# Optimization experiments

Hardware: AMD Instinct MI355X
Metric: run time of the kernel (lower is better)

## Reference

```python
import jax, jax.numpy as jnp
import numpy as np

D_MODEL = 2048
NUM_HEADS = 16
D_K = D_MODEL // NUM_HEADS
THETA = 10000.0
MAX_SEQ_LEN = 2048
B, S = 2, 2048


def setup_inputs() -> dict:
    key = jax.random.key(0)
    ks = jax.random.split(key, 5)
    x = jax.random.normal(ks[0], (B, S, D_MODEL), dtype=jnp.float32)
    token_positions = jnp.tile(jnp.arange(S, dtype=jnp.int64 if jax.config.jax_enable_x64 else jnp.int32), (B, 1))
    wq = jax.random.normal(ks[1], (D_MODEL, D_MODEL), dtype=jnp.float32)
    wk = jax.random.normal(ks[2], (D_MODEL, D_MODEL), dtype=jnp.float32)
    wv = jax.random.normal(ks[3], (D_MODEL, D_MODEL), dtype=jnp.float32)
    wo = jax.random.normal(ks[4], (D_MODEL, D_MODEL), dtype=jnp.float32)
    return {"x": x, "token_positions": token_positions, "wq": wq, "wk": wk, "wv": wv, "wo": wo}


def _rope_tables():
    # inv freqs: exp(arange(0,d_k,2) * (-log(theta)/d_k))  -> [d_k/2]
    inv_freq = jnp.exp(jnp.arange(0, D_K, 2, dtype=jnp.float32) * (-np.log(THETA) / D_K))
    m = jnp.arange(MAX_SEQ_LEN, dtype=jnp.float32)[:, None]  # [L,1]
    ang = m * inv_freq[None, :]                               # [L, d_k/2]
    return jnp.cos(ang), jnp.sin(ang)


def _apply_rope(x, token_positions, cos_tab, sin_tab):
    # x: [B, H, S, d_k]; token_positions: [B, S]
    cos = cos_tab[token_positions][:, None, :, :]  # [B,1,S,d_k/2]
    sin = sin_tab[token_positions][:, None, :, :]
    xe = x[..., 0::2]
    xo = x[..., 1::2]
    re = xe * cos - xo * sin
    ro = xo * cos + xe * sin
    out = jnp.stack([re, ro], axis=-1).reshape(x.shape)
    return out


def reference(x, token_positions, wq, wk, wv, wo):
    b, s, _ = x.shape
    cos_tab, sin_tab = _rope_tables()

    def split_heads(t):  # [B,S,D] -> [B,H,S,d_k]
        return t.reshape(b, s, NUM_HEADS, D_K).transpose(0, 2, 1, 3)

    q = _apply_rope(split_heads(x @ wq), token_positions, cos_tab, sin_tab)
    k = _apply_rope(split_heads(x @ wk), token_positions, cos_tab, sin_tab)
    v = split_heads(x @ wv)

    scores = jnp.einsum("bhqd,bhkd->bhqk", q, k) / jnp.sqrt(jnp.float32(D_K))
    causal = jnp.tril(jnp.ones((s, s), dtype=bool))
    scores = jnp.where(causal[None, None], scores, jnp.float32(-1e9))
    attn = jax.nn.softmax(scores, axis=-1)
    out = jnp.einsum("bhqk,bhkd->bhqd", attn, v)
    out = out.transpose(0, 2, 1, 3).reshape(b, s, D_MODEL)
    return out @ wo
```

## Files before the change

kernel.cpp:

```cpp
#include <hip/hip_runtime.h>
#include <hip/hip_bf16.h>
#include <cstdio>

namespace {

constexpr int kSeq = 2048;
constexpr int kDModel = 2048;
constexpr int kHeads = 16;
constexpr int kDk = 128;
constexpr int kBatch = 2;
constexpr int kM = kBatch * kSeq;
constexpr float kQScale = 0.08838834764831845f;

typedef __bf16 bf16_t;
typedef __bf16 bf16x8 __attribute__((ext_vector_type(8)));
typedef __bf16 bf16x4 __attribute__((ext_vector_type(4)));
typedef float f32x4 __attribute__((ext_vector_type(4)));
typedef short s16x4 __attribute__((ext_vector_type(4)));

__device__ __forceinline__ f32x4 mfma32(bf16x8 a, bf16x8 b, f32x4 c) {
  return __builtin_amdgcn_mfma_f32_16x16x32_bf16(a, b, c, 0, 0, 0);
}

#if __has_builtin(__builtin_amdgcn_mfma_f32_16x16x16_bf16)
__device__ __forceinline__ f32x4 mfma16(bf16x4 a, bf16x4 b, f32x4 c) {
  return __builtin_amdgcn_mfma_f32_16x16x16_bf16(a, b, c, 0, 0, 0);
}
#else
__device__ __forceinline__ f32x4 mfma16(bf16x4 a, bf16x4 b, f32x4 c) {
  union U { bf16x4 b; s16x4 s; } ua, ub;
  ua.b = a; ub.b = b;
  return __builtin_amdgcn_mfma_f32_16x16x16bf16_1k(ua.s, ub.s, c, 0, 0, 0);
}
#endif

using gas_void = const __attribute__((address_space(1))) void;
using las_void = __attribute__((address_space(3))) void;

__device__ __forceinline__ void gload_lds16(const bf16_t* g, bf16_t* l) {
  __builtin_amdgcn_global_load_lds((gas_void*)g, (las_void*)l, 16, 0, 0);
}

__global__ void k_rope_table(float* __restrict__ cost, float* __restrict__ sint) {
  const int p = blockIdx.x;
  const int i = threadIdx.x;
  const double inv = exp(-(double)(2 * i) * 9.210340371976184 / 128.0);
  const double ang = (double)p * inv;
  cost[p * 64 + i] = (float)cos(ang);
  sint[p * 64 + i] = (float)sin(ang);
}

__global__ void k_split_x(const float* __restrict__ x, bf16_t* __restrict__ xh,
                          bf16_t* __restrict__ xl, int n) {
  const int idx = (blockIdx.x * blockDim.x + threadIdx.x) * 4;
  if (idx >= n) return;
  const float4 v = *(const float4*)(x + idx);
  const float vv[4] = {v.x, v.y, v.z, v.w};
  bf16x4 hv, lv;
#pragma unroll
  for (int j = 0; j < 4; ++j) {
    const bf16_t h = (bf16_t)vv[j];
    hv[j] = h;
    lv[j] = (bf16_t)(vv[j] - (float)h);
  }
  *(bf16x4*)(xh + idx) = hv;
  *(bf16x4*)(xl + idx) = lv;
}

__global__ void k_transpose_w(const float* __restrict__ w, bf16_t* __restrict__ wth,
                              bf16_t* __restrict__ wtl) {
  __shared__ float tile[32][33];
  const int bx = blockIdx.x * 32;
  const int by = blockIdx.y * 32;
  const int tx = threadIdx.x, ty = threadIdx.y;
#pragma unroll
  for (int i = 0; i < 32; i += 8)
    tile[ty + i][tx] = w[(size_t)(by + ty + i) * kDModel + bx + tx];
  __syncthreads();
#pragma unroll
  for (int i = 0; i < 32; i += 8) {
    const float v = tile[tx][ty + i];
    const size_t o = (size_t)(bx + ty + i) * kDModel + by + tx;
    const bf16_t h = (bf16_t)v;
    wth[o] = h;
    if (wtl) wtl[o] = (bf16_t)(v - (float)h);
  }
}

__global__ __launch_bounds__(512, 2) void k_gemmqk(
    const bf16_t* __restrict__ Ah, const bf16_t* __restrict__ Al,
    const bf16_t* __restrict__ Bh, const bf16_t* __restrict__ Bl,
    bf16_t* __restrict__ Qh, bf16_t* __restrict__ Ql,
    bf16_t* __restrict__ Kh, bf16_t* __restrict__ Kl,
    const int* __restrict__ tokpos, const float* __restrict__ cost,
    const float* __restrict__ sint) {
  __shared__ __align__(16) bf16_t sA[3][512 * 32];
  __shared__ __align__(16) bf16_t sB[3][128 * 32];
  constexpr int ntk = 192;

  const int tid = threadIdx.x;
  const int wid = tid >> 6, lane = tid & 63;
  const int lo = lane & 15, hi = lane >> 4;
  const int wr = wid >> 1, wc = wid & 1;

  const int bid = blockIdx.x;
  const int wgid = (bid & 7) * 32 + (bid >> 3);
  const int mt = wgid >> 5, nt = wgid & 31;
  const int m0 = mt * 512, n0 = nt * 128;

  const int sr = tid >> 2;
  const int sc = ((tid & 3) ^ ((sr >> 1) & 3)) * 8;
  size_t offA[4];
#pragma unroll
  for (int ui = 0; ui < 4; ++ui)
    offA[ui] = (size_t)(m0 + ui * 128 + sr) * 2048 + sc;
  const size_t offB = (size_t)(n0 + sr) * 2048 + sc;
  const int ldsT = wid * 512;

  auto STAGE = [&](int slot, int tt) {
    const bf16_t *As, *Bs;
    int kb;
    if (tt < 64) {
      As = Ah; Bs = Bh; kb = tt * 32;
    } else if (tt < 128) {
      As = Ah; Bs = Bl; kb = (tt - 64) * 32;
    } else {
      As = Al; Bs = Bh; kb = (tt - 128) * 32;
    }
    bf16_t* dA = sA[slot] + ldsT;
#pragma unroll
    for (int ui = 0; ui < 4; ++ui)
      gload_lds16(As + offA[ui] + kb, dA + ui * 4096);
    gload_lds16(Bs + offB + kb, sB[slot] + ldsT);
  };

  const int xq = (lo >> 1) & 3;
  int aoff[8], boff[4];
#pragma unroll
  for (int mi = 0; mi < 8; ++mi)
    aoff[mi] = (wr * 128 + mi * 16 + lo) * 32 + ((hi ^ xq) * 8);
#pragma unroll
  for (int ni = 0; ni < 4; ++ni)
    boff[ni] = (wc * 64 + ni * 16 + lo) * 32 + ((hi ^ xq) * 8);

  f32x4 acc[8][4];
  const f32x4 z = {0.f, 0.f, 0.f, 0.f};
#pragma unroll
  for (int i = 0; i < 8; ++i)
#pragma unroll
    for (int j = 0; j < 4; ++j) acc[i][j] = z;

  STAGE(0, 0);
  STAGE(1, 1);
  asm volatile("s_waitcnt vmcnt(5)" ::: "memory");
  __builtin_amdgcn_s_barrier();
  __builtin_amdgcn_sched_barrier(0);

  int s0 = 0;
#pragma unroll 1
  for (int t = 0; t < ntk; ++t) {
    const bf16_t* sa = sA[s0];
    const bf16_t* sb = sB[s0];
    int s2 = s0 + 2;
    if (s2 >= 3) s2 -= 3;

    bf16x8 af[8], bfr[4];
#pragma unroll
    for (int mi = 0; mi < 4; ++mi) af[mi] = *(const bf16x8*)(sa + aoff[mi]);
#pragma unroll
    for (int ni = 0; ni < 4; ++ni) bfr[ni] = *(const bf16x8*)(sb + boff[ni]);
    if (t + 2 < ntk) STAGE(s2, t + 2);
#pragma unroll
    for (int mi = 4; mi < 8; ++mi) af[mi] = *(const bf16x8*)(sa + aoff[mi]);

    if (t + 3 < ntk)
      asm volatile("s_waitcnt vmcnt(5)" ::: "memory");
    else
      asm volatile("s_waitcnt vmcnt(0)" ::: "memory");
    asm volatile("s_waitcnt lgkmcnt(4)" ::: "memory");
    __builtin_amdgcn_s_barrier();
    __builtin_amdgcn_sched_barrier(0);

    __builtin_amdgcn_s_setprio(1);
#pragma unroll
    for (int ni = 0; ni < 4; ++ni)
#pragma unroll
      for (int mi = 0; mi < 4; ++mi)
        acc[mi][ni] = mfma32(af[mi], bfr[ni], acc[mi][ni]);
    __builtin_amdgcn_s_setprio(0);

    asm volatile("s_waitcnt lgkmcnt(0)" ::: "memory");
    __builtin_amdgcn_sched_barrier(0);
    __builtin_amdgcn_s_setprio(1);
#pragma unroll
    for (int ni = 0; ni < 4; ++ni)
#pragma unroll
      for (int mi = 4; mi < 8; ++mi)
        acc[mi][ni] = mfma32(af[mi], bfr[ni], acc[mi][ni]);
    __builtin_amdgcn_s_setprio(0);

    __builtin_amdgcn_s_barrier();
    __builtin_amdgcn_sched_barrier(0);

    s0 += 1;
    if (s0 >= 3) s0 = 0;
  }

  const int qk = n0 >> 11;
  bf16_t* Xh = qk ? Kh : Qh;
  bf16_t* Xl = qk ? Kl : Ql;
  const float scale = qk ? 1.0f : kQScale;
  const int is64 = (tokpos[1] == 0) ? 1 : 0;
#pragma unroll
  for (int mi = 0; mi < 8; ++mi) {
#pragma unroll
    for (int r = 0; r < 4; ++r) {
      const int row = m0 + wr * 128 + mi * 16 + hi * 4 + r;
      const int pos = is64 ? tokpos[2 * row] : tokpos[row];
#pragma unroll
      for (int ni = 0; ni < 4; ++ni) {
        const int col = n0 + wc * 64 + ni * 16 + lo;
        const float v = acc[mi][ni][r] * scale;
        const float pv = __shfl_xor(v, 1);
        const int ip = (col & 127) >> 1;
        const float c = cost[pos * 64 + ip];
        const float sn = sint[pos * 64 + ip];
        const float sgn = (lo & 1) ? sn : -sn;
        const float rv = v * c + pv * sgn;
        const bf16_t hb = (bf16_t)rv;
        const size_t o = (size_t)row * 2048 + (col & 2047);
        Xh[o] = hb;
        Xl[o] = (bf16_t)(rv - (float)hb);
      }
    }
  }
}

template <int EPI>
__global__ __launch_bounds__(512) void k_gemm8(
    const bf16_t* __restrict__ Ah, const bf16_t* __restrict__ Bh,
    void* __restrict__ O0, int NT, int ntk) {
  __shared__ __align__(16) bf16_t sA[3][256 * 64];
  __shared__ __align__(16) bf16_t sB[3][128 * 64];

  const int tid = threadIdx.x;
  const int wid = tid >> 6, lane = tid & 63;
  const int lo = lane & 15, hi = lane >> 4;
  const int wrr = wid >> 1, wcc = wid & 1;
  const int x7 = lo & 7;

  const int bid = blockIdx.x;
  const int wgid = (bid & 7) * (gridDim.x >> 3) + (bid >> 3);
  const int mt = wgid / NT, nt = wgid % NT;
  const int m0 = mt * 256, n0 = nt * 128;

  const int rB = tid >> 3;
  const int ch8 = ((tid & 7) ^ (rB & 7)) * 8;
  size_t offA[4], offB[2];
#pragma unroll
  for (int u = 0; u < 2; ++u)
#pragma unroll
    for (int i = 0; i < 2; ++i)
      offA[u * 2 + i] = (size_t)(m0 + u * 128 + i * 64 + rB) * 2048 + ch8;
#pragma unroll
  for (int i = 0; i < 2; ++i)
    offB[i] = (size_t)(n0 + i * 64 + rB) * 2048 + ch8;
  const int ldsOff = wid * 512;

  auto STAGE_A = [&](int slot, int t) {
    const bf16_t* base = Ah + t * 64;
    bf16_t* d = sA[slot] + ldsOff;
#pragma unroll
    for (int ui = 0; ui < 4; ++ui) gload_lds16(base + offA[ui], d + ui * 4096);
  };
  auto STAGE_B = [&](int slot, int t) {
    const bf16_t* base = Bh + t * 64;
    bf16_t* d = sB[slot] + ldsOff;
#pragma unroll
    for (int i = 0; i < 2; ++i) gload_lds16(base + offB[i], d + i * 4096);
  };

  int aoff[4][2], boff[4][2];
#pragma unroll
  for (int mi = 0; mi < 4; ++mi)
#pragma unroll
    for (int ks = 0; ks < 2; ++ks)
      aoff[mi][ks] = (wrr * 64 + mi * 16 + lo) * 64 + (((ks * 4 + hi) ^ x7) * 8);
#pragma unroll
  for (int ni = 0; ni < 4; ++ni)
#pragma unroll
    for (int ks = 0; ks < 2; ++ks)
      boff[ni][ks] = (wcc * 64 + ni * 16 + lo) * 64 + (((ks * 4 + hi) ^ x7) * 8);

  f32x4 acc[4][4];
  const f32x4 z = {0.f, 0.f, 0.f, 0.f};
#pragma unroll
  for (int i = 0; i < 4; ++i)
#pragma unroll
    for (int j = 0; j < 4; ++j) acc[i][j] = z;

  STAGE_A(0, 0);
  STAGE_B(0, 0);
  STAGE_A(1, 1);
  STAGE_B(1, 1);
  asm volatile("s_waitcnt vmcnt(6)" ::: "memory");
  __builtin_amdgcn_s_barrier();
  asm volatile("" ::: "memory");

  int s0 = 0;
  for (int t = 0; t < ntk; ++t) {
    const bf16_t* sa = sA[s0];
    const bf16_t* sb = sB[s0];
    int s2 = s0 + 2;
    if (s2 >= 3) s2 -= 3;
    const bool pf = (t + 2 < ntk);

    bf16x8 af[2][2], bfr[4][2];
#pragma unroll
    for (int mi = 0; mi < 2; ++mi)
#pragma unroll
      for (int ks = 0; ks < 2; ++ks)
        af[mi][ks] = *(const bf16x8*)(sa + aoff[mi][ks]);
#pragma unroll
    for (int ni = 0; ni < 4; ++ni)
#pragma unroll
      for (int ks = 0; ks < 2; ++ks)
        bfr[ni][ks] = *(const bf16x8*)(sb + boff[ni][ks]);
    if (pf) STAGE_A(s2, t + 2);
    asm volatile("" ::: "memory");
    __builtin_amdgcn_s_barrier();
    asm volatile("" ::: "memory");
    __builtin_amdgcn_s_setprio(1);
#pragma unroll
    for (int ni = 0; ni < 4; ++ni)
#pragma unroll
      for (int mi = 0; mi < 2; ++mi)
#pragma unroll
        for (int ks = 0; ks < 2; ++ks)
          acc[mi][ni] = mfma32(af[mi][ks], bfr[ni][ks], acc[mi][ni]);
    __builtin_amdgcn_s_setprio(0);

    bf16x8 ag[2][2];
#pragma unroll
    for (int mi = 0; mi < 2; ++mi)
#pragma unroll
      for (int ks = 0; ks < 2; ++ks)
        ag[mi][ks] = *(const bf16x8*)(sa + aoff[2 + mi][ks]);
    if (pf) STAGE_B(s2, t + 2);
    if (pf)
      asm volatile("s_waitcnt vmcnt(6)" ::: "memory");
    else
      asm volatile("s_waitcnt vmcnt(0)" ::: "memory");
    __builtin_amdgcn_s_barrier();
    asm volatile("" ::: "memory");
    __builtin_amdgcn_s_setprio(1);
#pragma unroll
    for (int ni = 0; ni < 4; ++ni)
#pragma unroll
      for (int mi = 0; mi < 2; ++mi)
#pragma unroll
        for (int ks = 0; ks < 2; ++ks)
          acc[2 + mi][ni] = mfma32(ag[mi][ks], bfr[ni][ks], acc[2 + mi][ni]);
    __builtin_amdgcn_s_setprio(0);

    s0 += 1;
    if (s0 >= 3) s0 = 0;
  }

  if constexpr (EPI == 0) {
    float* C = (float*)O0;
#pragma unroll
    for (int mi = 0; mi < 4; ++mi)
#pragma unroll
      for (int ni = 0; ni < 4; ++ni)
#pragma unroll
        for (int r = 0; r < 4; ++r) {
          const int row = m0 + wrr * 64 + mi * 16 + hi * 4 + r;
          const int col = n0 + wcc * 64 + ni * 16 + lo;
          C[(size_t)row * 2048 + col] = acc[mi][ni][r];
        }
  } else {
    bf16_t* VT = (bf16_t*)O0;
#pragma unroll
    for (int mi = 0; mi < 4; ++mi)
#pragma unroll
      for (int ni = 0; ni < 4; ++ni) {
        const int col = n0 + wcc * 64 + ni * 16 + lo;
        const int h = col >> 7, d = col & 127;
        const int rowb = m0 + wrr * 64 + mi * 16 + hi * 4;
        const int b = rowb >> 11, s = rowb & (kSeq - 1);
        bf16x4 ov;
#pragma unroll
        for (int r = 0; r < 4; ++r) ov[r] = (bf16_t)acc[mi][ni][r];
        *(bf16x4*)(VT + ((size_t)((b * kHeads + h) * kDk + d)) * kSeq + s) = ov;
      }
  }
}

__global__ __launch_bounds__(512, 2) void k_attn4(
    const bf16_t* __restrict__ Qh, const bf16_t* __restrict__ Ql,
    const bf16_t* __restrict__ Kh, const bf16_t* __restrict__ Kl,
    const bf16_t* __restrict__ VT, bf16_t* __restrict__ Ob) {
  __shared__ __align__(16) bf16_t sK[2][2][64 * 128];
  __shared__ __align__(16) bf16_t sV[2][128 * 64];

  const int tid = threadIdx.x;
  const int wid = tid >> 6, lane = tid & 63;
  const int lo = lane & 15, hi = lane >> 4;
  const int flat = blockIdx.x;
  const int j = flat >> 3;
  const int bh = (flat & 7) * 4 + (j & 3);
  const int p = j >> 2;
  const int b = bh >> 4, h = bh & 15;
  const int qiW = (wid < 4) ? (15 - p) : p;
  const int qw = qiW * 128 + (wid & 3) * 32;
  const int nkv = 2 * (15 - p) + 2;

  bf16x8 qhf[4][2], qlf[4][2];
  {
    const size_t qbase =
        (size_t)(b * kSeq + qw + lo) * kDModel + h * kDk + hi * 8;
#pragma unroll
    for (int qt = 0; qt < 2; ++qt)
#pragma unroll
      for (int ks = 0; ks < 4; ++ks) {
        const size_t o = qbase + (size_t)qt * 16 * kDModel + ks * 32;
        qhf[ks][qt] = *(const bf16x8*)(Qh + o);
        qlf[ks][qt] = *(const bf16x8*)(Ql + o);
      }
  }

  const int rK0 = wid * 8 + (lane >> 4);
  const int gK0 = ((lane & 15) ^ (rK0 & 15)) * 8;
  const int gK1 = ((lane & 15) ^ ((rK0 + 4) & 15)) * 8;
  const bf16_t* pKh0 = Kh + (size_t)(b * kSeq + rK0) * kDModel + h * kDk + gK0;
  const bf16_t* pKh1 = Kh + (size_t)(b * kSeq + rK0 + 4) * kDModel + h * kDk + gK1;
  const bf16_t* pKl0 = Kl + (pKh0 - Kh);
  const bf16_t* pKl1 = Kl + (pKh1 - Kh);
  const int dV0 = wid * 16 + (lane >> 3);
  const int gV0 = ((lane & 7) ^ (dV0 & 7)) * 8;
  const int gV1 = ((lane & 7) ^ ((dV0 + 8) & 7)) * 8;
  const bf16_t* pV0 = VT + (size_t)(bh * kDk + dV0) * kSeq + gV0;
  const bf16_t* pV1 = VT + (size_t)(bh * kDk + dV0 + 8) * kSeq + gV1;
  const int ldsK = (wid * 8) * 128;
  const int ldsV = (wid * 16) * 64;

  f32x4 of[8][2];
  const f32x4 z = {0.f, 0.f, 0.f, 0.f};
#pragma unroll
  for (int di = 0; di < 8; ++di) {
    of[di][0] = z;
    of[di][1] = z;
  }
  float m[2] = {-3e38f, -3e38f};
  float l[2] = {0.f, 0.f};

  auto STAGE = [&](int buf, int t) {
    const size_t ko = (size_t)t * 64 * kDModel;
    const size_t vo = (size_t)t * 64;
    bf16_t* dk = sK[buf][0] + ldsK;
    bf16_t* dl = sK[buf][1] + ldsK;
    gload_lds16(pKh0 + ko, dk);
    gload_lds16(pKh1 + ko, dk + 512);
    gload_lds16(pKl0 + ko, dl);
    gload_lds16(pKl1 + ko, dl + 512);
    bf16_t* dv = sV[buf] + ldsV;
    gload_lds16(pV0 + vo, dv);
    gload_lds16(pV1 + vo, dv + 512);
  };

  STAGE(0, 0);
  __syncthreads();

  for (int t = 0; t < nkv; ++t) {
    const int kv0 = t * 64;
    if (t + 1 < nkv) STAGE((t + 1) & 1, t + 1);

    if (kv0 <= qw + 31) {
      const bf16_t* bKh = sK[t & 1][0];
      const bf16_t* bKl = sK[t & 1][1];
      const bf16_t* bV = sV[t & 1];
      const bool maskedw = (kv0 + 63 > qw);

      f32x4 st[4][2];
#pragma unroll
      for (int kt = 0; kt < 4; ++kt) {
        st[kt][0] = z;
        st[kt][1] = z;
      }
#pragma unroll
      for (int kt = 0; kt < 4; ++kt) {
#pragma unroll
        for (int ks = 0; ks < 4; ++ks) {
          const int krow = kt * 16 + lo;
          const int ka = krow * 128 + (((ks * 4 + hi) ^ (krow & 15)) * 8);
          const bf16x8 kh8 = *(const bf16x8*)(bKh + ka);
          const bf16x8 kl8 = *(const bf16x8*)(bKl + ka);
#pragma unroll
          for (int qt = 0; qt < 2; ++qt) {
            st[kt][qt] = mfma32(kh8, qhf[ks][qt], st[kt][qt]);
            st[kt][qt] = mfma32(kh8, qlf[ks][qt], st[kt][qt]);
            st[kt][qt] = mfma32(kl8, qhf[ks][qt], st[kt][qt]);
          }
        }
      }

      bf16x4 pb[4][2];
#pragma unroll
      for (int qt = 0; qt < 2; ++qt) {
        const int q = qw + qt * 16 + lo;
        float mt = -3e38f;
#pragma unroll
        for (int kt = 0; kt < 4; ++kt)
#pragma unroll
          for (int r = 0; r < 4; ++r) {
            float s = st[kt][qt][r];
            if (maskedw && (kv0 + kt * 16 + hi * 4 + r > q)) s = -1e30f;
            st[kt][qt][r] = s;
            mt = fmaxf(mt, s);
          }
        mt = fmaxf(mt, __shfl_xor(mt, 16));
        mt = fmaxf(mt, __shfl_xor(mt, 32));
        if (!__all(mt <= m[qt] + 8.f)) {
          const float mnew = fmaxf(m[qt], mt);
          const float corr = __expf(m[qt] - mnew);
          l[qt] *= corr;
#pragma unroll
          for (int di = 0; di < 8; ++di) of[di][qt] = of[di][qt] * corr;
          m[qt] = mnew;
        }
        float rs = 0.f;
#pragma unroll
        for (int kt = 0; kt < 4; ++kt) {
          bf16x4 pv;
#pragma unroll
          for (int r = 0; r < 4; ++r) {
            const float pp = __expf(st[kt][qt][r] - m[qt]);
            rs += pp;
            pv[r] = (bf16_t)pp;
          }
          pb[kt][qt] = pv;
        }
        rs += __shfl_xor(rs, 16);
        rs += __shfl_xor(rs, 32);
        l[qt] += rs;
      }

#pragma unroll
      for (int di = 0; di < 8; ++di) {
        const int d = di * 16 + lo;
#pragma unroll
        for (int kt = 0; kt < 4; ++kt) {
          const int va =
              d * 64 + (((kt * 2 + (hi >> 1)) ^ (d & 7)) * 8) + (hi & 1) * 4;
          const bf16x4 vf = *(const bf16x4*)(bV + va);
          of[di][0] = mfma16(vf, pb[kt][0], of[di][0]);
          of[di][1] = mfma16(vf, pb[kt][1], of[di][1]);
        }
      }
    }
    __syncthreads();
  }

#pragma unroll
  for (int qt = 0; qt < 2; ++qt) {
    const float linv = 1.f / l[qt];
    const size_t ob =
        (size_t)(b * kSeq + qw + qt * 16 + lo) * kDModel + h * kDk + hi * 4;
#pragma unroll
    for (int di = 0; di < 8; ++di) {
      bf16x4 ov;
#pragma unroll
      for (int r = 0; r < 4; ++r) ov[r] = (bf16_t)(of[di][qt][r] * linv);
      *(bf16x4*)(Ob + ob + di * 16) = ov;
    }
  }
}

}

extern "C" void kernel_launch(void* const* d_in, const int* in_sizes, int n_in,
                              void* d_out, int out_size, void* d_ws, size_t ws_size,
                              hipStream_t stream) {
  (void)in_sizes; (void)n_in; (void)out_size;
  const float* x = (const float*)d_in[0];
  const int* tokpos = (const int*)d_in[1];
  const float* wq = (const float*)d_in[2];
  const float* wk = (const float*)d_in[3];
  const float* wv = (const float*)d_in[4];
  const float* wo = (const float*)d_in[5];
  float* out = (float*)d_out;

  char* p = (char*)d_ws;
  auto take = [&](size_t bytes) { char* q = p; p += bytes; return q; };
  float* cost = (float*)take((size_t)kSeq * 64 * sizeof(float));
  float* sint = (float*)take((size_t)kSeq * 64 * sizeof(float));
  const size_t mat = (size_t)kM * kDModel * sizeof(bf16_t);
  const size_t wmat = (size_t)kDModel * kDModel * sizeof(bf16_t);
  bf16_t* xh = (bf16_t*)take(mat);
  bf16_t* xl = (bf16_t*)take(mat);
  bf16_t* wqkth = (bf16_t*)take(2 * wmat);
  bf16_t* wqktl = (bf16_t*)take(2 * wmat);
  bf16_t* wvt = (bf16_t*)take(wmat);
  bf16_t* wot = (bf16_t*)take(wmat);
  bf16_t* qh = (bf16_t*)take(mat);
  bf16_t* ql = (bf16_t*)take(mat);
  bf16_t* kh = (bf16_t*)take(mat);
  bf16_t* kl = (bf16_t*)take(mat);
  bf16_t* vt = (bf16_t*)take(mat);
  bf16_t* ob = (bf16_t*)take(mat);
  if ((size_t)(p - (char*)d_ws) > ws_size) {
    fprintf(stderr, "MHA: workspace too small: need %zu have %zu\n",
            (size_t)(p - (char*)d_ws), ws_size);
    return;
  }

  k_rope_table<<<dim3(kSeq), dim3(64), 0, stream>>>(cost, sint);
  k_split_x<<<dim3((kM * kDModel) / (256 * 4)), dim3(256), 0, stream>>>(
      x, xh, xl, kM * kDModel);
  {
    dim3 tb(32, 8), tg(kDModel / 32, kDModel / 32);
    k_transpose_w<<<tg, tb, 0, stream>>>(wq, wqkth, wqktl);
    k_transpose_w<<<tg, tb, 0, stream>>>(wk, wqkth + (size_t)2048 * 2048,
                                         wqktl + (size_t)2048 * 2048);
    k_transpose_w<<<tg, tb, 0, stream>>>(wv, wvt, nullptr);
    k_transpose_w<<<tg, tb, 0, stream>>>(wo, wot, nullptr);
  }
  k_gemmqk<<<dim3(256), dim3(512), 0, stream>>>(xh, xl, wqkth, wqktl, qh, ql,
                                                kh, kl, tokpos, cost, sint);
  k_gemm8<2><<<dim3(256), dim3(512), 0, stream>>>(xh, wvt, vt, 16, 32);
  k_attn4<<<dim3(256), dim3(512), 0, stream>>>(qh, ql, kh, kl, vt, ob);
  k_gemm8<0><<<dim3(256), dim3(512), 0, stream>>>(ob, wot, out, 16, 32);
}
```

Before: 502.9 us.

## Reshape fused QK GEMM tile to 256x256 and split staging across compute halves

The fused Q/K projection GEMM changes its block tile from 512x128 to 256x256, with a 2x4 wave layout instead of 4x2. Global-to-LDS staging is split into separate A and B prefetches that are interleaved between the two MFMA halves of each k-step. This is meant to spread memory issue more evenly across the loop and shrink the LDS footprint. It adds extra barriers per iteration, drops the occupancy hint from the launch bounds, and needs care with the vmcnt accounting near the end of the loop.

```diff
diff --git a/kernel.cpp b/kernel.cpp
--- a/kernel.cpp
+++ b/kernel.cpp
@@ -87,51 +87,49 @@
   }
 }
 
-__global__ __launch_bounds__(512, 2) void k_gemmqk(
+__global__ __launch_bounds__(512) void k_gemmf(
     const bf16_t* __restrict__ Ah, const bf16_t* __restrict__ Al,
     const bf16_t* __restrict__ Bh, const bf16_t* __restrict__ Bl,
     bf16_t* __restrict__ Qh, bf16_t* __restrict__ Ql,
     bf16_t* __restrict__ Kh, bf16_t* __restrict__ Kl,
     const int* __restrict__ tokpos, const float* __restrict__ cost,
     const float* __restrict__ sint) {
-  __shared__ __align__(16) bf16_t sA[3][512 * 32];
-  __shared__ __align__(16) bf16_t sB[3][128 * 32];
+  __shared__ __align__(16) bf16_t sA[3][256 * 32];
+  __shared__ __align__(16) bf16_t sB[3][256 * 32];
   constexpr int ntk = 192;
 
   const int tid = threadIdx.x;
   const int wid = tid >> 6, lane = tid & 63;
   const int lo = lane & 15, hi = lane >> 4;
-  const int wr = wid >> 1, wc = wid & 1;
+  const int wr = wid >> 2;
+  const int wc = wid & 3;
 
   const int bid = blockIdx.x;
   const int wgid = (bid & 7) * 32 + (bid >> 3);
-  const int mt = wgid >> 5, nt = wgid & 31;
-  const int m0 = mt * 512, n0 = nt * 128;
+  const int m0 = (wgid >> 4) * 256, n0 = (wgid & 15) * 256;
 
   const int sr = tid >> 2;
-  const int sc = ((tid & 3) ^ ((sr >> 1) & 3)) * 8;
-  size_t offA[4];
-#pragma unroll
-  for (int ui = 0; ui < 4; ++ui)
-    offA[ui] = (size_t)(m0 + ui * 128 + sr) * 2048 + sc;
-  const size_t offB = (size_t)(n0 + sr) * 2048 + sc;
-  const int ldsT = wid * 512;
-
-  auto STAGE = [&](int slot, int tt) {
-    const bf16_t *As, *Bs;
-    int kb;
-    if (tt < 64) {
-      As = Ah; Bs = Bh; kb = tt * 32;
-    } else if (tt < 128) {
-      As = Ah; Bs = Bl; kb = (tt - 64) * 32;
-    } else {
-      As = Al; Bs = Bh; kb = (tt - 128) * 32;
-    }
-    bf16_t* dA = sA[slot] + ldsT;
-#pragma unroll
-    for (int ui = 0; ui < 4; ++ui)
-      gload_lds16(As + offA[ui] + kb, dA + ui * 4096);
-    gload_lds16(Bs + offB + kb, sB[slot] + ldsT);
+  const int sc = ((tid & 3) ^ ((tid >> 3) & 3)) * 8;
+  size_t offA[2], offB[2];
+#pragma unroll
+  for (int i = 0; i < 2; ++i) {
+    offA[i] = (size_t)(m0 + i * 128 + sr) * 2048 + sc;
+    offB[i] = (size_t)(n0 + i * 128 + sr) * 2048 + sc;
+  }
+
+  auto STAGE_A = [&](int slot, int tt) {
+    const bf16_t* As = (tt < 128) ? Ah : Al;
+    const int kb = (tt & 63) * 32;
+#pragma unroll
+    for (int i = 0; i < 2; ++i)
+      gload_lds16(As + offA[i] + kb, sA[slot] + i * 4096 + tid * 8);
+  };
+  auto STAGE_B = [&](int slot, int tt) {
+    const bf16_t* Bs = (tt < 64) ? Bh : ((tt < 128) ? Bl : Bh);
+    const int kb = (tt & 63) * 32;
+#pragma unroll
+    for (int i = 0; i < 2; ++i)
+      gload_lds16(Bs + offB[i] + kb, sB[slot] + i * 4096 + tid * 8);
   };
 
   const int xq = (lo >> 1) & 3;
@@ -150,9 +148,11 @@
 #pragma unroll
     for (int j = 0; j < 4; ++j) acc[i][j] = z;
 
-  STAGE(0, 0);
-  STAGE(1, 1);
-  asm volatile("s_waitcnt vmcnt(5)" ::: "memory");
+  STAGE_A(0, 0);
+  STAGE_B(0, 0);
+  STAGE_A(1, 1);
+  STAGE_B(1, 1);
+  asm volatile("s_waitcnt vmcnt(4)" ::: "memory");
   __builtin_amdgcn_s_barrier();
   __builtin_amdgcn_sched_barrier(0);
 
@@ -163,42 +163,49 @@
     const bf16_t* sb = sB[s0];
     int s2 = s0 + 2;
     if (s2 >= 3) s2 -= 3;
-
-    bf16x8 af[8], bfr[4];
-#pragma unroll
-    for (int mi = 0; mi < 4; ++mi) af[mi] = *(const bf16x8*)(sa + aoff[mi]);
-#pragma unroll
-    for (int ni = 0; ni < 4; ++ni) bfr[ni] = *(const bf16x8*)(sb + boff[ni]);
-    if (t + 2 < ntk) STAGE(s2, t + 2);
-#pragma unroll
-    for (int mi = 4; mi < 8; ++mi) af[mi] = *(const bf16x8*)(sa + aoff[mi]);
-
-    if (t + 3 < ntk)
-      asm volatile("s_waitcnt vmcnt(5)" ::: "memory");
-    else
+    const bool pf = (t + 2 < ntk);
+
+    bf16x8 a[4], b[4];
+#pragma unroll
+    for (int mi = 0; mi < 4; ++mi) a[mi] = *(const bf16x8*)(sa + aoff[mi]);
+#pragma unroll
+    for (int ni = 0; ni < 4; ++ni) b[ni] = *(const bf16x8*)(sb + boff[ni]);
+    if (pf) STAGE_A(s2, t + 2);
+    __builtin_amdgcn_sched_barrier(0);
+    __builtin_amdgcn_s_barrier();
+    asm volatile("s_waitcnt lgkmcnt(0)" ::: "memory");
+    __builtin_amdgcn_sched_barrier(0);
+    __builtin_amdgcn_s_setprio(1);
+#pragma unroll
+    for (int ni = 0; ni < 4; ++ni)
+#pragma unroll
+      for (int mi = 0; mi < 4; ++mi)
+        acc[mi][ni] = mfma32(a[mi], b[ni], acc[mi][ni]);
+    __builtin_amdgcn_s_setprio(0);
+    __builtin_amdgcn_sched_barrier(0);
+    __builtin_amdgcn_s_barrier();
+    __builtin_amdgcn_sched_barrier(0);
+
+    bf16x8 a2[4];
+#pragma unroll
+    for (int mi = 0; mi < 4; ++mi) a2[mi] = *(const bf16x8*)(sa + aoff[4 + mi]);
+    if (pf) STAGE_B(s2, t + 2);
+    __builtin_amdgcn_sched_barrier(0);
+    if (pf)
+      asm volatile("s_waitcnt vmcnt(4)" ::: "memory");
+    else if (t == ntk - 2)
       asm volatile("s_waitcnt vmcnt(0)" ::: "memory");
-    asm volatile("s_waitcnt lgkmcnt(4)" ::: "memory");
     __builtin_amdgcn_s_barrier();
-    __builtin_amdgcn_sched_barrier(0);
-
+    asm volatile("s_waitcnt lgkmcnt(0)" ::: "memory");
+    __builtin_amdgcn_sched_barrier(0);
     __builtin_amdgcn_s_setprio(1);
 #pragma unroll
     for (int ni = 0; ni < 4; ++ni)
 #pragma unroll
       for (int mi = 0; mi < 4; ++mi)
-        acc[mi][ni] = mfma32(af[mi], bfr[ni], acc[mi][ni]);
+        acc[4 + mi][ni] = mfma32(a2[mi], b[ni], acc[4 + mi][ni]);
     __builtin_amdgcn_s_setprio(0);
-
-    asm volatile("s_waitcnt lgkmcnt(0)" ::: "memory");
-    __builtin_amdgcn_sched_barrier(0);
-    __builtin_amdgcn_s_setprio(1);
-#pragma unroll
-    for (int ni = 0; ni < 4; ++ni)
-#pragma unroll
-      for (int mi = 4; mi < 8; ++mi)
-        acc[mi][ni] = mfma32(af[mi], bfr[ni], acc[mi][ni]);
-    __builtin_amdgcn_s_setprio(0);
-
+    __builtin_amdgcn_sched_barrier(0);
     __builtin_amdgcn_s_barrier();
     __builtin_amdgcn_sched_barrier(0);
 
@@ -626,8 +633,8 @@
     k_transpose_w<<<tg, tb, 0, stream>>>(wv, wvt, nullptr);
     k_transpose_w<<<tg, tb, 0, stream>>>(wo, wot, nullptr);
   }
-  k_gemmqk<<<dim3(256), dim3(512), 0, stream>>>(xh, xl, wqkth, wqktl, qh, ql,
-                                                kh, kl, tokpos, cost, sint);
+  k_gemmf<<<dim3(256), dim3(512), 0, stream>>>(xh, xl, wqkth, wqktl, qh, ql,
+                                               kh, kl, tokpos, cost, sint);
   k_gemm8<2><<<dim3(256), dim3(512), 0, stream>>>(xh, wvt, vt, 16, 32);
   k_attn4<<<dim3(256), dim3(512), 0, stream>>>(qh, ql, kh, kl, vt, ob);
   k_gemm8<0><<<dim3(256), dim3(512), 0, stream>>>(ob, wot, out, 16, 32);
```

New measurement: 421.5 us. -16.2%, faster.
